# Kernel optimization log

Hardware: AMD Instinct MI355X
Metric: run time of the kernel (lower is better)

The kernel has to match this reference:

```python
import jax, jax.numpy as jnp
import numpy as np

B = 4
MAX_N = 2048
D = 512
H = 8
HD = D // H
SRC_LENS = [2048, 1536, 1800, 1200]   # sum = 6584
REF_LENS = [1900, 2048, 1400, 1600]   # sum = 6948
NEG_INF = -1e9


def setup_inputs() -> dict:
    key = jax.random.key(0)
    ks = jax.random.split(key, 8)
    n_src, n_ref = sum(SRC_LENS), sum(REF_LENS)
    s = 0.02
    return {
        "feats_src": jax.random.normal(ks[0], (n_src, D), dtype=jnp.float32),
        "batch_src": jnp.asarray(np.repeat(np.arange(B), SRC_LENS), dtype=jnp.int32),
        "feats_ref": jax.random.normal(ks[1], (n_ref, D), dtype=jnp.float32),
        "batch_ref": jnp.asarray(np.repeat(np.arange(B), REF_LENS), dtype=jnp.int32),
        "w_in": jax.random.normal(ks[2], (3 * D, D), dtype=jnp.float32) * s,
        "b_in": jnp.zeros((3 * D,), dtype=jnp.float32),
        "w_out": jax.random.normal(ks[3], (D, D), dtype=jnp.float32) * s,
        "b_out": jnp.zeros((D,), dtype=jnp.float32),
        "gw1": jax.random.normal(ks[4], (D, D), dtype=jnp.float32) * s,
        "gb1": jnp.zeros((D,), dtype=jnp.float32),
        "gw2": jax.random.normal(ks[5], (1, D), dtype=jnp.float32) * s,
        "gb2": jnp.zeros((1,), dtype=jnp.float32),
    }


def _to_dense(feats, batch_idx):
    # sparse [N, D] (sorted batch indices) -> dense [B, MAX_N, D] + key_padding_mask
    n = feats.shape[0]
    counts = jax.ops.segment_sum(jnp.ones((n,), jnp.int32), batch_idx, num_segments=B)
    starts = jnp.concatenate([jnp.zeros((1,), jnp.int32), jnp.cumsum(counts)[:-1].astype(jnp.int32)])
    pos = jnp.arange(n, dtype=jnp.int32) - starts[batch_idx]  # position within batch
    dense = jnp.zeros((B, MAX_N, feats.shape[1]), feats.dtype).at[batch_idx, pos].set(feats)
    mask = jnp.arange(MAX_N)[None, :] >= counts[:, None]  # True = padding (key_padding_mask)
    return dense, mask, pos


def reference(feats_src, batch_src, feats_ref, batch_ref,
              w_in, b_in, w_out, b_out, gw1, gb1, gw2, gb2):
    d_src, mask_src, pos_src = _to_dense(feats_src, batch_src)
    d_ref, mask_ref, _ = _to_dense(feats_ref, batch_ref)

    # nn.MultiheadAttention (batch_first, eval mode): packed in_proj, scaled dot-product
    q = (d_src @ w_in[:D].T + b_in[:D]).reshape(B, MAX_N, H, HD)
    k = (d_ref @ w_in[D:2 * D].T + b_in[D:2 * D]).reshape(B, MAX_N, H, HD)
    v = (d_ref @ w_in[2 * D:].T + b_in[2 * D:]).reshape(B, MAX_N, H, HD)
    scores = jnp.einsum('bqhd,bkhd->bhqk', q * (HD ** -0.5), k)
    scores = jnp.where(mask_ref[:, None, None, :], NEG_INF, scores)
    attn = jax.nn.softmax(scores, axis=-1)
    ctx = jnp.einsum('bhqk,bkhd->bqhd', attn, v).reshape(B, MAX_N, D)
    d_aligned = ctx @ w_out.T + b_out

    # gate MLP: Linear -> ReLU -> Linear -> Sigmoid
    gate = jax.nn.sigmoid(jax.nn.relu(d_aligned @ gw1.T + gb1) @ gw2.T + gb2)  # [B, MAX_N, 1]
    d_out = d_src + gate * d_aligned

    # dense -> ragged: gather each token back to its flat slot
    out_flat = d_out[batch_src, pos_src]  # [N_src, D]
    return out_flat, gate
```

## Files before the change

### kernel.cpp

```cpp
#include <hip/hip_runtime.h>
#include <hip/hip_bf16.h>


typedef __bf16 bf16x8_t __attribute__((ext_vector_type(8)));
typedef __bf16 bf16x4_t __attribute__((ext_vector_type(4)));
typedef float f32x4_t __attribute__((ext_vector_type(4)));
typedef float f32x2_t __attribute__((ext_vector_type(2)));

#define CQ_SCALE 0.18033688011112042f

__device__ inline bf16x8_t zero8() {
  bf16x8_t z;
#pragma unroll
  for (int t = 0; t < 8; ++t) z[t] = (__bf16)0.0f;
  return z;
}

__device__ __forceinline__ int sniff_f32(const void* w) {
  unsigned short u = ((const unsigned short*)w)[threadIdx.x & 63];
  return __ballot((u & 0x7F80) >= 0x3F80) != 0ULL;
}

__global__ void sentinel_k(float* out) {
  if (threadIdx.x == 0 && blockIdx.x == 0) out[0] = 1000.0f;
}

__global__ void cv_all(const void* w_in, const void* b_in, const void* w_out,
                       const void* b_out, const void* gw1, const void* gb1,
                       const void* gw2, const void* gb2,
                       __hip_bfloat16* __restrict__ ws) {
  int f = sniff_f32(w_in);
  const size_t F_W_IN = 16, F_B_IN = 786448, F_W_OUT = 787984, F_B_OUT = 1050128,
               F_GW1 = 1050640, F_GB1 = 1312784, F_GW2 = 1313296, F_GB2 = 1313808;
  const int total = 1313793;
  for (int g = blockIdx.x * 256 + threadIdx.x; g < total; g += gridDim.x * 256) {
    const void* src;
    size_t dst;
    int i;
    if (g < 786432) { src = w_in; dst = F_W_IN; i = g; }
    else if (g < 787968) { src = b_in; dst = F_B_IN; i = g - 786432; }
    else if (g < 1050112) { src = w_out; dst = F_W_OUT; i = g - 787968; }
    else if (g < 1050624) { src = b_out; dst = F_B_OUT; i = g - 1050112; }
    else if (g < 1312768) { src = gw1; dst = F_GW1; i = g - 1050624; }
    else if (g < 1313280) { src = gb1; dst = F_GB1; i = g - 1312768; }
    else if (g < 1313792) { src = gw2; dst = F_GW2; i = g - 1313280; }
    else { src = gb2; dst = F_GB2; i = g - 1313792; }
    ws[dst + i] = f ? __float2bfloat16(((const float*)src)[i])
                    : ((const __hip_bfloat16*)src)[i];
  }
}

__device__ __forceinline__ void gemm_core(
    const void* __restrict__ A_, long aoff, const __hip_bfloat16* __restrict__ Bt,
    const __hip_bfloat16* __restrict__ bias, __hip_bfloat16* __restrict__ C,
    int M, int K, int lda, int ldc, float cscale, int relu, int f, int bm, int bn,
    __bf16 (&As)[128][64], __bf16 (&Bs)[128][64]) {
  int tid = threadIdx.x, lane = tid & 63, wave = tid >> 6;
  int wm = wave >> 1, wn = wave & 1;
  int l15 = lane & 15, quad = lane >> 4;

  f32x4_t acc[4][4];
#pragma unroll
  for (int i = 0; i < 4; ++i)
#pragma unroll
    for (int j = 0; j < 4; ++j)
#pragma unroll
      for (int r = 0; r < 4; ++r) acc[i][j][r] = 0.f;

  bf16x8_t ra[4], rb[4];
  f32x4_t raf[4][2];

  auto gload = [&](int k0) {
#pragma unroll
    for (int s = 0; s < 4; ++s) {
      int id = s * 256 + tid;
      int row = id >> 3, col = (id & 7) * 8;
      int arow = bm + row;
      if (f) {
        if (arow < M) {
          const float* p = (const float*)A_ + aoff + (size_t)arow * lda + k0 + col;
          raf[s][0] = *reinterpret_cast<const f32x4_t*>(p);
          raf[s][1] = *reinterpret_cast<const f32x4_t*>(p + 4);
        } else {
#pragma unroll
          for (int e = 0; e < 4; ++e) { raf[s][0][e] = 0.f; raf[s][1][e] = 0.f; }
        }
      } else {
        ra[s] = (arow < M)
                    ? *reinterpret_cast<const bf16x8_t*>((const __hip_bfloat16*)A_ + aoff +
                                                         (size_t)arow * lda + k0 + col)
                    : zero8();
      }
      rb[s] = *reinterpret_cast<const bf16x8_t*>(Bt + (size_t)(bn + row) * 512 + k0 + col);
    }
  };
  auto stage = [&]() {
#pragma unroll
    for (int s = 0; s < 4; ++s) {
      int id = s * 256 + tid;
      int row = id >> 3, col = (id & 7) * 8;
      if (f) {
        bf16x8_t t;
#pragma unroll
        for (int e = 0; e < 4; ++e) {
          t[e] = (__bf16)raf[s][0][e];
          t[4 + e] = (__bf16)raf[s][1][e];
        }
        *reinterpret_cast<bf16x8_t*>(&As[row][col]) = t;
      } else {
        *reinterpret_cast<bf16x8_t*>(&As[row][col]) = ra[s];
      }
      *reinterpret_cast<bf16x8_t*>(&Bs[row][col]) = rb[s];
    }
  };

  int nk = K >> 6;
  gload(0);
  for (int it = 0; it < nk; ++it) {
    stage();
    __syncthreads();
    if (it + 1 < nk) gload((it + 1) * 64);
#pragma unroll
    for (int ks = 0; ks < 2; ++ks) {
      bf16x8_t af[4], bfv[4];
#pragma unroll
      for (int i = 0; i < 4; ++i)
        af[i] = *reinterpret_cast<const bf16x8_t*>(
            &As[wm * 64 + i * 16 + l15][ks * 32 + quad * 8]);
#pragma unroll
      for (int j = 0; j < 4; ++j)
        bfv[j] = *reinterpret_cast<const bf16x8_t*>(
            &Bs[wn * 64 + j * 16 + l15][ks * 32 + quad * 8]);
#pragma unroll
      for (int i = 0; i < 4; ++i)
#pragma unroll
        for (int j = 0; j < 4; ++j)
          acc[i][j] = __builtin_amdgcn_mfma_f32_16x16x32_bf16(af[i], bfv[j], acc[i][j], 0, 0, 0);
    }
    __syncthreads();
  }

#pragma unroll
  for (int i = 0; i < 4; ++i)
#pragma unroll
    for (int j = 0; j < 4; ++j) {
      int col = bn + wn * 64 + j * 16 + l15;
      float bv = __bfloat162float(bias[col]);
#pragma unroll
      for (int r = 0; r < 4; ++r) {
        int row = bm + wm * 64 + i * 16 + quad * 4 + r;
        if (row < M) {
          float v = (acc[i][j][r] + bv) * cscale;
          if (relu) v = fmaxf(v, 0.f);
          C[(size_t)row * ldc + col] = __float2bfloat16(v);
        }
      }
    }
}

__global__ __launch_bounds__(256) void proj2(
    const void* __restrict__ fs, const void* __restrict__ fr,
    const __hip_bfloat16* __restrict__ ws, __hip_bfloat16* __restrict__ Q,
    __hip_bfloat16* __restrict__ KV, const void* snf) {
  __shared__ __bf16 As[128][64];
  __shared__ __bf16 Bs[128][64];
  const size_t F_W_IN = 16, F_B_IN = 786448;
  int f = sniff_f32(snf);
  int bid = blockIdx.x;
  if (bid < 208) {
    int bx = bid >> 2, by = bid & 3;
    gemm_core(fs, 0, ws + F_W_IN, ws + F_B_IN, Q, 6584, 512, 512, 512, CQ_SCALE, 0, f,
              bx * 128, by * 128, As, Bs);
  } else {
    int k = bid - 208;
    int bx = k >> 3, by = k & 7;
    gemm_core(fr, 0, ws + F_W_IN + 262144, ws + F_B_IN + 512, KV, 6948, 512, 512, 1024,
              1.0f, 0, f, bx * 128, by * 128, As, Bs);
  }
}

template <bool AF32>
__global__ __launch_bounds__(256) void gemm128(
    const void* __restrict__ A_, long aoff, const __hip_bfloat16* __restrict__ Bt,
    const __hip_bfloat16* __restrict__ bias, __hip_bfloat16* __restrict__ C,
    int M, int K, int lda, int ldc, float cscale, int relu, const void* snf) {
  __shared__ __bf16 As[128][64];
  __shared__ __bf16 Bs[128][64];
  int f = 0;
  if constexpr (AF32) f = sniff_f32(snf);
  gemm_core(A_, aoff, Bt, bias, C, M, K, lda, ldc, cscale, relu, f,
            blockIdx.x * 128, blockIdx.y * 128, As, Bs);
}

__global__ __launch_bounds__(256) void gemm128_pv(
    const __hip_bfloat16* __restrict__ P0, const __hip_bfloat16* __restrict__ P1,
    const float* __restrict__ L, const __hip_bfloat16* __restrict__ Bt,
    const __hip_bfloat16* __restrict__ bias, __hip_bfloat16* __restrict__ C,
    int M) {
  __shared__ __bf16 As[128][64];
  __shared__ __bf16 Bs[128][64];
  int tid = threadIdx.x, lane = tid & 63, wave = tid >> 6;
  int wm = wave >> 1, wn = wave & 1;
  int l15 = lane & 15, quad = lane >> 4;
  int bm = blockIdx.x * 128, bn = blockIdx.y * 128;

  f32x4_t acc[4][4];
#pragma unroll
  for (int i = 0; i < 4; ++i)
#pragma unroll
    for (int j = 0; j < 4; ++j)
#pragma unroll
      for (int r = 0; r < 4; ++r) acc[i][j][r] = 0.f;

  bf16x8_t rp0[4], rp1[4], rb[4];
  f32x2_t rl[4];

  auto gload = [&](int k0) {
    int h = k0 >> 6;
#pragma unroll
    for (int s = 0; s < 4; ++s) {
      int id = s * 256 + tid;
      int row = id >> 3, col = (id & 7) * 8;
      int arow = bm + row;
      if (arow < M) {
        size_t off = (size_t)arow * 512 + k0 + col;
        rp0[s] = *reinterpret_cast<const bf16x8_t*>(P0 + off);
        rp1[s] = *reinterpret_cast<const bf16x8_t*>(P1 + off);
        rl[s] = *reinterpret_cast<const f32x2_t*>(&L[((size_t)arow * 8 + h) * 2]);
      } else {
        rp0[s] = zero8();
        rp1[s] = zero8();
        rl[s][0] = 1.f;
        rl[s][1] = 0.f;
      }
      rb[s] = *reinterpret_cast<const bf16x8_t*>(Bt + (size_t)(bn + row) * 512 + k0 + col);
    }
  };
  auto stage = [&]() {
#pragma unroll
    for (int s = 0; s < 4; ++s) {
      int id = s * 256 + tid;
      int row = id >> 3, col = (id & 7) * 8;
      float sc = 1.0f / (rl[s][0] + rl[s][1]);
      float w0 = rl[s][0] * sc, w1 = rl[s][1] * sc;
      bf16x8_t t;
#pragma unroll
      for (int e = 0; e < 8; ++e)
        t[e] = (__bf16)(w0 * (float)rp0[s][e] + w1 * (float)rp1[s][e]);
      *reinterpret_cast<bf16x8_t*>(&As[row][col]) = t;
      *reinterpret_cast<bf16x8_t*>(&Bs[row][col]) = rb[s];
    }
  };

  gload(0);
  for (int it = 0; it < 8; ++it) {
    stage();
    __syncthreads();
    if (it + 1 < 8) gload((it + 1) * 64);
#pragma unroll
    for (int ks = 0; ks < 2; ++ks) {
      bf16x8_t af[4], bfv[4];
#pragma unroll
      for (int i = 0; i < 4; ++i)
        af[i] = *reinterpret_cast<const bf16x8_t*>(
            &As[wm * 64 + i * 16 + l15][ks * 32 + quad * 8]);
#pragma unroll
      for (int j = 0; j < 4; ++j)
        bfv[j] = *reinterpret_cast<const bf16x8_t*>(
            &Bs[wn * 64 + j * 16 + l15][ks * 32 + quad * 8]);
#pragma unroll
      for (int i = 0; i < 4; ++i)
#pragma unroll
        for (int j = 0; j < 4; ++j)
          acc[i][j] = __builtin_amdgcn_mfma_f32_16x16x32_bf16(af[i], bfv[j], acc[i][j], 0, 0, 0);
    }
    __syncthreads();
  }

#pragma unroll
  for (int i = 0; i < 4; ++i)
#pragma unroll
    for (int j = 0; j < 4; ++j) {
      int col = bn + wn * 64 + j * 16 + l15;
      float bv = __bfloat162float(bias[col]);
#pragma unroll
      for (int r = 0; r < 4; ++r) {
        int row = bm + wm * 64 + i * 16 + quad * 4 + r;
        if (row < M)
          C[(size_t)row * 512 + col] = __float2bfloat16(acc[i][j][r] + bv);
      }
    }
}

__device__ __forceinline__ void flash_core(
    const __hip_bfloat16* __restrict__ Qb, const __hip_bfloat16* __restrict__ KVb,
    __hip_bfloat16* __restrict__ OUTb, float* __restrict__ LPb, int nsrc, int nref,
    int qt, int kt0, int ktNfull, int do_tail,
    __bf16 (&VtL)[2][64][72], __bf16 (&PL)[4][32][72]) {
  int h = blockIdx.y;
  int tid = threadIdx.x, lane = tid & 63, wave = tid >> 6;
  int l15 = lane & 15, quad = lane >> 4;
  int Mb = nsrc + 1;
  int qbase = qt * 128 + wave * 32;

  bf16x8_t qfr[2][2];
#pragma unroll
  for (int g = 0; g < 2; ++g) {
    int qrow = qbase + g * 16 + l15;
#pragma unroll
    for (int ks = 0; ks < 2; ++ks)
      qfr[g][ks] = (qrow < nsrc)
                       ? *reinterpret_cast<const bf16x8_t*>(
                             Qb + (size_t)qrow * 512 + h * 64 + ks * 32 + quad * 8)
                       : zero8();
  }

  f32x4_t O[2][4];
#pragma unroll
  for (int g = 0; g < 2; ++g)
#pragma unroll
    for (int j = 0; j < 4; ++j)
#pragma unroll
      for (int r = 0; r < 4; ++r) O[g][j][r] = 0.f;

  f32x4_t Lacc[2];
#pragma unroll
  for (int g = 0; g < 2; ++g)
#pragma unroll
    for (int r = 0; r < 4; ++r) Lacc[g][r] = 0.f;
  bf16x8_t ones;
#pragma unroll
  for (int t = 0; t < 8; ++t) ones[t] = (__bf16)1.0f;

  bf16x8_t kf[8], v0, v1;
  auto loadK = [&](int k0) {
#pragma unroll
    for (int j = 0; j < 4; ++j) {
      const __hip_bfloat16* kp =
          KVb + (size_t)(k0 + j * 16 + l15) * 1024 + h * 64 + quad * 8;
      kf[j * 2] = *reinterpret_cast<const bf16x8_t*>(kp);
      kf[j * 2 + 1] = *reinterpret_cast<const bf16x8_t*>(kp + 32);
    }
  };
  auto loadV = [&](int k0) {
    const __hip_bfloat16* vp = KVb + (size_t)(k0 + lane) * 1024 + 512 + h * 64 + wave * 16;
    v0 = *reinterpret_cast<const bf16x8_t*>(vp);
    v1 = *reinterpret_cast<const bf16x8_t*>(vp + 8);
  };

  int nit = ktNfull - kt0;
  if (nit > 0) {
    loadK(kt0 * 64);
    loadV(kt0 * 64);
  }

  for (int it = 0; it < nit; ++it) {
    int k0 = (kt0 + it) * 64;
    __bf16(*Vt)[72] = VtL[it & 1];
#pragma unroll
    for (int e = 0; e < 8; ++e) {
      Vt[wave * 16 + e][lane] = v0[e];
      Vt[wave * 16 + 8 + e][lane] = v1[e];
    }
    if (it + 1 < nit) loadV(k0 + 64);

#pragma unroll
    for (int g = 0; g < 2; ++g) {
      f32x4_t St[4];
#pragma unroll
      for (int j = 0; j < 4; ++j)
#pragma unroll
        for (int r = 0; r < 4; ++r) St[j][r] = 0.f;
#pragma unroll
      for (int j = 0; j < 4; ++j)
#pragma unroll
        for (int ks = 0; ks < 2; ++ks)
          St[j] = __builtin_amdgcn_mfma_f32_16x16x32_bf16(kf[j * 2 + ks], qfr[g][ks],
                                                          St[j], 0, 0, 0);
#pragma unroll
      for (int j = 0; j < 4; ++j) {
        bf16x4_t pk;
#pragma unroll
        for (int r = 0; r < 4; ++r) pk[r] = (__bf16)exp2f(St[j][r]);
        *reinterpret_cast<bf16x4_t*>(&PL[wave][g * 16 + l15][j * 16 + quad * 4]) = pk;
      }
    }
    if (it + 1 < nit) loadK(k0 + 64);

    __syncthreads();

    bf16x8_t pa[2][2];
#pragma unroll
    for (int g = 0; g < 2; ++g)
#pragma unroll
      for (int ks = 0; ks < 2; ++ks)
        pa[g][ks] = *reinterpret_cast<const bf16x8_t*>(
            &PL[wave][g * 16 + l15][ks * 32 + quad * 8]);
#pragma unroll
    for (int g = 0; g < 2; ++g)
#pragma unroll
      for (int ks = 0; ks < 2; ++ks)
        Lacc[g] = __builtin_amdgcn_mfma_f32_16x16x32_bf16(pa[g][ks], ones, Lacc[g], 0, 0, 0);
#pragma unroll
    for (int j = 0; j < 4; ++j)
#pragma unroll
      for (int ks = 0; ks < 2; ++ks) {
        bf16x8_t vbf =
            *reinterpret_cast<const bf16x8_t*>(&Vt[j * 16 + l15][ks * 32 + quad * 8]);
#pragma unroll
        for (int g = 0; g < 2; ++g)
          O[g][j] = __builtin_amdgcn_mfma_f32_16x16x32_bf16(pa[g][ks], vbf, O[g][j], 0, 0, 0);
      }
  }

  if (do_tail) {
    int k0 = ktNfull * 64;
    __bf16(*Vt)[72] = VtL[nit & 1];
    {
      int kr = k0 + lane;
      const __hip_bfloat16* vp = KVb + (size_t)kr * 1024 + 512 + h * 64 + wave * 16;
      bf16x8_t t0 = (kr < nref) ? *reinterpret_cast<const bf16x8_t*>(vp) : zero8();
      bf16x8_t t1 = (kr < nref) ? *reinterpret_cast<const bf16x8_t*>(vp + 8) : zero8();
#pragma unroll
      for (int e = 0; e < 8; ++e) {
        Vt[wave * 16 + e][lane] = t0[e];
        Vt[wave * 16 + 8 + e][lane] = t1[e];
      }
    }
#pragma unroll
    for (int j = 0; j < 4; ++j) {
      int kcol = k0 + j * 16 + l15;
      const __hip_bfloat16* kp = KVb + (size_t)kcol * 1024 + h * 64 + quad * 8;
      kf[j * 2] = (kcol < nref) ? *reinterpret_cast<const bf16x8_t*>(kp) : zero8();
      kf[j * 2 + 1] = (kcol < nref) ? *reinterpret_cast<const bf16x8_t*>(kp + 32) : zero8();
    }
#pragma unroll
    for (int g = 0; g < 2; ++g) {
      f32x4_t St[4];
#pragma unroll
      for (int j = 0; j < 4; ++j)
#pragma unroll
        for (int r = 0; r < 4; ++r) St[j][r] = 0.f;
#pragma unroll
      for (int j = 0; j < 4; ++j)
#pragma unroll
        for (int ks = 0; ks < 2; ++ks)
          St[j] = __builtin_amdgcn_mfma_f32_16x16x32_bf16(kf[j * 2 + ks], qfr[g][ks],
                                                          St[j], 0, 0, 0);
#pragma unroll
      for (int j = 0; j < 4; ++j) {
        bf16x4_t pk;
#pragma unroll
        for (int r = 0; r < 4; ++r) {
          int kl = k0 + j * 16 + quad * 4 + r;
          pk[r] = (__bf16)((kl < nref) ? exp2f(St[j][r]) : 0.f);
        }
        *reinterpret_cast<bf16x4_t*>(&PL[wave][g * 16 + l15][j * 16 + quad * 4]) = pk;
      }
    }
    __syncthreads();
    bf16x8_t pa[2][2];
#pragma unroll
    for (int g = 0; g < 2; ++g)
#pragma unroll
      for (int ks = 0; ks < 2; ++ks)
        pa[g][ks] = *reinterpret_cast<const bf16x8_t*>(
            &PL[wave][g * 16 + l15][ks * 32 + quad * 8]);
#pragma unroll
    for (int g = 0; g < 2; ++g)
#pragma unroll
      for (int ks = 0; ks < 2; ++ks)
        Lacc[g] = __builtin_amdgcn_mfma_f32_16x16x32_bf16(pa[g][ks], ones, Lacc[g], 0, 0, 0);
#pragma unroll
    for (int j = 0; j < 4; ++j)
#pragma unroll
      for (int ks = 0; ks < 2; ++ks) {
        bf16x8_t vbf =
            *reinterpret_cast<const bf16x8_t*>(&Vt[j * 16 + l15][ks * 32 + quad * 8]);
#pragma unroll
        for (int g = 0; g < 2; ++g)
          O[g][j] = __builtin_amdgcn_mfma_f32_16x16x32_bf16(pa[g][ks], vbf, O[g][j], 0, 0, 0);
      }
  }

  if (LPb && l15 == 0) {
#pragma unroll
    for (int g = 0; g < 2; ++g)
#pragma unroll
      for (int r = 0; r < 4; ++r) {
        int row = qbase + g * 16 + quad * 4 + r;
        if (row < Mb) LPb[((size_t)row * 8 + h) * 2] = Lacc[g][r];
      }
  }

#pragma unroll
  for (int g = 0; g < 2; ++g)
#pragma unroll
    for (int r = 0; r < 4; ++r) {
      int row = qbase + g * 16 + quad * 4 + r;
      if (row < Mb) {
        float inv = 1.0f / Lacc[g][r];
#pragma unroll
        for (int j = 0; j < 4; ++j)
          OUTb[(size_t)row * 512 + h * 64 + j * 16 + l15] =
              __float2bfloat16(O[g][j][r] * inv);
      }
    }
}

__global__ __launch_bounds__(256, 3) void flash_all(
    const __hip_bfloat16* __restrict__ Q, const __hip_bfloat16* __restrict__ KV,
    __hip_bfloat16* __restrict__ O0, __hip_bfloat16* __restrict__ O1,
    float* __restrict__ L, int nsplit) {
  const int TILE_START[4] = {0, 17, 30, 45};
  const int SRC_START[4] = {0, 2048, 3584, 5384};
  const int REF_START[4] = {0, 1900, 3948, 5348};
  const int SRC_LEN[4] = {2048, 1536, 1800, 1200};
  const int REF_LEN[4] = {1900, 2048, 1400, 1600};
  const int CS[4] = {0, 2049, 3586, 5387};
  __shared__ __bf16 VtL[2][64][72];
  __shared__ __bf16 PL[4][32][72];
  int bid = blockIdx.x;
  int b = (bid >= TILE_START[3]) ? 3 : (bid >= TILE_START[2]) ? 2 : (bid >= TILE_START[1]) ? 1 : 0;
  int qt = bid - TILE_START[b];
  int nref = REF_LEN[b];
  int full = nref >> 6, nkt = (nref + 63) >> 6, rem = nref & 63;
  int split = blockIdx.z;
  int kt0, ktN, tail;
  if (nsplit == 1) { kt0 = 0; ktN = full; tail = rem > 0; }
  else if (split == 0) { int half = nkt >> 1; kt0 = 0; ktN = half; tail = 0; }
  else { int half = nkt >> 1; kt0 = half; ktN = full; tail = rem > 0; }
  __hip_bfloat16* OUT = (nsplit == 1 || split == 0) ? O0 : O1;
  float* LP = (nsplit == 1) ? nullptr : (L + split + (size_t)CS[b] * 16);
  flash_core(Q + (size_t)SRC_START[b] * 512, KV + (size_t)REF_START[b] * 1024,
             OUT + (size_t)CS[b] * 512, LP, SRC_LEN[b], nref, qt, kt0, ktN, tail, VtL, PL);
}

__global__ __launch_bounds__(256, 3) void flash_one(const __hip_bfloat16* __restrict__ Qb,
                                                    const __hip_bfloat16* __restrict__ KVb,
                                                    __hip_bfloat16* __restrict__ OUTb,
                                                    int nsrc, int nref) {
  __shared__ __bf16 VtL[2][64][72];
  __shared__ __bf16 PL[4][32][72];
  flash_core(Qb, KVb, OUTb, nullptr, nsrc, nref, blockIdx.x, 0, nref >> 6,
             (nref & 63) > 0, VtL, PL);
}

__global__ __launch_bounds__(256) void finalize_all(
    const void* __restrict__ src, const __hip_bfloat16* __restrict__ aligned,
    const __hip_bfloat16* __restrict__ hidden, const __hip_bfloat16* __restrict__ gw2,
    const __hip_bfloat16* __restrict__ gb2, void* __restrict__ out, const void* snf) {
  int f = sniff_f32(snf);
  int lane = threadIdx.x & 63;
  int r = blockIdx.x * 4 + (threadIdx.x >> 6);
  int b = (r >= 5387) ? 3 : (r >= 3586) ? 2 : (r >= 2049) ? 1 : 0;
  const int CS[4] = {0, 2049, 3586, 5387};
  const int NSRC[4] = {2048, 1536, 1800, 1200};
  int pos = r - CS[b];

  float zacc = 0.f;
  const __hip_bfloat16* hrow = hidden + (size_t)r * 512;
#pragma unroll
  for (int t = 0; t < 8; ++t) {
    int c = lane + (t << 6);
    zacc += __bfloat162float(hrow[c]) * __bfloat162float(gw2[c]);
  }
  for (int o = 32; o; o >>= 1) zacc += __shfl_xor(zacc, o);
  zacc += __bfloat162float(gb2[0]);
  float g = 1.f / (1.f + __expf(-zacc));

  const size_t GOFF = (size_t)6584 * 512;
  if (pos < NSRC[b]) {
    size_t ib = (size_t)(r - b) * 512;
    const __hip_bfloat16* arow = aligned + (size_t)r * 512;
#pragma unroll
    for (int t = 0; t < 8; ++t) {
      int c = lane + (t << 6);
      float sv = f ? ((const float*)src)[ib + c]
                   : __bfloat162float(((const __hip_bfloat16*)src)[ib + c]);
      float val = sv + g * __bfloat162float(arow[c]);
      if (f) ((float*)out)[ib + c] = val;
      else ((__hip_bfloat16*)out)[ib + c] = __float2bfloat16(val);
    }
    if (lane == 0) {
      size_t go = GOFF + b * 2048 + pos;
      if (f) ((float*)out)[go] = g;
      else ((__hip_bfloat16*)out)[go] = __float2bfloat16(g);
    }
  } else {
    for (int p = NSRC[b] + lane; p < 2048; p += 64) {
      size_t go = GOFF + b * 2048 + p;
      if (f) ((float*)out)[go] = g;
      else ((__hip_bfloat16*)out)[go] = __float2bfloat16(g);
    }
  }
}

__global__ __launch_bounds__(256) void finalize_b(
    const void* __restrict__ src, const __hip_bfloat16* __restrict__ alnb,
    const __hip_bfloat16* __restrict__ hidb, const __hip_bfloat16* __restrict__ gw2,
    const __hip_bfloat16* __restrict__ gb2, void* __restrict__ out,
    int b, int nsrc, int src_start, const void* snf) {
  int f = sniff_f32(snf);
  int lane = threadIdx.x & 63;
  int r = blockIdx.x * 4 + (threadIdx.x >> 6);
  if (r > nsrc) return;

  float zacc = 0.f;
  const __hip_bfloat16* hrow = hidb + (size_t)r * 512;
#pragma unroll
  for (int t = 0; t < 8; ++t) {
    int c = lane + (t << 6);
    zacc += __bfloat162float(hrow[c]) * __bfloat162float(gw2[c]);
  }
  for (int o = 32; o; o >>= 1) zacc += __shfl_xor(zacc, o);
  zacc += __bfloat162float(gb2[0]);
  float g = 1.f / (1.f + __expf(-zacc));

  const size_t GOFF = (size_t)6584 * 512;
  if (r < nsrc) {
    size_t ib = (size_t)(src_start + r) * 512;
    const __hip_bfloat16* arow = alnb + (size_t)r * 512;
#pragma unroll
    for (int t = 0; t < 8; ++t) {
      int c = lane + (t << 6);
      float sv = f ? ((const float*)src)[ib + c]
                   : __bfloat162float(((const __hip_bfloat16*)src)[ib + c]);
      float val = sv + g * __bfloat162float(arow[c]);
      if (f) ((float*)out)[ib + c] = val;
      else ((__hip_bfloat16*)out)[ib + c] = __float2bfloat16(val);
    }
    if (lane == 0) {
      size_t go = GOFF + b * 2048 + r;
      if (f) ((float*)out)[go] = g;
      else ((__hip_bfloat16*)out)[go] = __float2bfloat16(g);
    }
  } else {
    for (int p = nsrc + lane; p < 2048; p += 64) {
      size_t go = GOFF + b * 2048 + p;
      if (f) ((float*)out)[go] = g;
      else ((__hip_bfloat16*)out)[go] = __float2bfloat16(g);
    }
  }
}

extern "C" void kernel_launch(void* const* d_in, const int* in_sizes, int n_in,
                              void* d_out, int out_size, void* d_ws, size_t ws_size,
                              hipStream_t stream) {
  (void)in_sizes; (void)n_in; (void)out_size;
  const void* feats_src = d_in[0];
  const void* feats_ref = d_in[2];
  const void* w_in = d_in[4];
  const void* b_in = d_in[5];
  const void* w_out = d_in[6];
  const void* b_out = d_in[7];
  const void* gw1 = d_in[8];
  const void* gb1 = d_in[9];
  const void* gw2 = d_in[10];
  const void* gb2 = d_in[11];

  const size_t F_W_IN = 16, F_B_IN = 786448, F_W_OUT = 787984, F_B_OUT = 1050128,
               F_GW1 = 1050640, F_GB1 = 1312784, F_GW2 = 1313296, F_GB2 = 1313808,
               A0 = 1313824;
  const size_t NEED_A2 = 2 * 22139936;
  const size_t NEED_A = 2 * 15178784;
  const size_t NEED_B = 2 * (A0 + 4259840);

  if (ws_size < NEED_B) {
    sentinel_k<<<1, 64, 0, stream>>>((float*)d_out);
    return;
  }

  __hip_bfloat16* ws = (__hip_bfloat16*)d_ws;
  cv_all<<<dim3(1024), dim3(256), 0, stream>>>(w_in, b_in, w_out, b_out, gw1, gb1, gw2,
                                               gb2, ws);

  const int SRC_LEN[4] = {2048, 1536, 1800, 1200};
  const int REF_LEN[4] = {1900, 2048, 1400, 1600};
  const int SRC_START[4] = {0, 2048, 3584, 5384};
  const int REF_START[4] = {0, 1900, 3948, 5348};
  dim3 blk(256);

  if (ws_size >= NEED_A) {
    __hip_bfloat16* R1 = ws + A0;
    __hip_bfloat16* R2 = R1 + 3375104;
    __hip_bfloat16* R3 = R2 + 7114752;
    proj2<<<dim3(648), blk, 0, stream>>>(feats_src, feats_ref, ws, R1, R2, w_in);
    if (ws_size >= NEED_A2) {
      __hip_bfloat16* P0 = R3 + 3375104;
      __hip_bfloat16* P1 = P0 + 3375104;
      float* L = (float*)(ws + 21928992);
      flash_all<<<dim3(55, 8, 2), blk, 0, stream>>>(R1, R2, P0, P1, L, 2);
      gemm128_pv<<<dim3(52, 4), blk, 0, stream>>>(P0, P1, L, ws + F_W_OUT, ws + F_B_OUT,
                                                  R1, 6588);
    } else {
      flash_all<<<dim3(55, 8, 1), blk, 0, stream>>>(R1, R2, R3, nullptr, nullptr, 1);
      gemm128<false><<<dim3(52, 4), blk, 0, stream>>>(R3, 0, ws + F_W_OUT, ws + F_B_OUT,
                                                      R1, 6588, 512, 512, 512, 1.0f, 0,
                                                      nullptr);
    }
    gemm128<false><<<dim3(52, 4), blk, 0, stream>>>(R1, 0, ws + F_GW1, ws + F_GB1, R3,
                                                    6588, 512, 512, 512, 1.0f, 1,
                                                    nullptr);
    finalize_all<<<dim3(1647), blk, 0, stream>>>(feats_src, R1, R3, ws + F_GW2,
                                                 ws + F_GB2, d_out, w_in);
  } else {
    __hip_bfloat16* W2 = ws + A0;
    __hip_bfloat16* W1 = W2 + 2097152;
    __hip_bfloat16* W3 = W1 + 1081344;
    for (int b = 0; b < 4; ++b) {
      int nsrc = SRC_LEN[b], nref = REF_LEN[b];
      gemm128<true><<<dim3((nsrc + 127) / 128, 4), blk, 0, stream>>>(
          feats_src, (long)SRC_START[b] * 512, ws + F_W_IN, ws + F_B_IN, W1, nsrc, 512,
          512, 512, CQ_SCALE, 0, w_in);
      gemm128<true><<<dim3((nref + 127) / 128, 8), blk, 0, stream>>>(
          feats_ref, (long)REF_START[b] * 512, ws + F_W_IN + 262144, ws + F_B_IN + 512,
          W2, nref, 512, 512, 1024, 1.0f, 0, w_in);
      flash_one<<<dim3((nsrc + 128) / 128, 8), blk, 0, stream>>>(W1, W2, W3, nsrc, nref);
      gemm128<false><<<dim3((nsrc + 128) / 128, 4), blk, 0, stream>>>(
          W3, 0, ws + F_W_OUT, ws + F_B_OUT, W1, nsrc + 1, 512, 512, 512, 1.0f, 0,
          nullptr);
      gemm128<false><<<dim3((nsrc + 128) / 128, 4), blk, 0, stream>>>(
          W1, 0, ws + F_GW1, ws + F_GB1, W3, nsrc + 1, 512, 512, 512, 1.0f, 1, nullptr);
      finalize_b<<<dim3((nsrc + 4) / 4), blk, 0, stream>>>(
          feats_src, W1, W3, ws + F_GW2, ws + F_GB2, d_out, b, nsrc, SRC_START[b], w_in);
    }
  }
}
```

Measured before the change: 256.6 us.

## Generalize flash-decoding KV split to four splits with templated merge GEMM

Flash attention now splits the key range into NS parts (4 when workspace allows, else 2 or 1), writing partial outputs and row sums into contiguous slabs. The out-projection GEMM is templated on NS and merges the partial outputs, weighted by their row sums, while staging its A tile. Launch bounds on the flash kernels rise from 3 to 4 waves per SIMD to raise occupancy. More splits add parallelism (55x8x4 blocks), but they also add partial-output traffic and merge work, and register pressure may spill under the tighter launch bound.

```diff
diff --git a/kernel.cpp b/kernel.cpp
--- a/kernel.cpp
+++ b/kernel.cpp
@@ -192,11 +192,12 @@
             blockIdx.x * 128, blockIdx.y * 128, As, Bs);
 }
 
+template <int NS>
 __global__ __launch_bounds__(256) void gemm128_pv(
-    const __hip_bfloat16* __restrict__ P0, const __hip_bfloat16* __restrict__ P1,
-    const float* __restrict__ L, const __hip_bfloat16* __restrict__ Bt,
-    const __hip_bfloat16* __restrict__ bias, __hip_bfloat16* __restrict__ C,
-    int M) {
+    const __hip_bfloat16* __restrict__ P, const float* __restrict__ L,
+    const __hip_bfloat16* __restrict__ Bt, const __hip_bfloat16* __restrict__ bias,
+    __hip_bfloat16* __restrict__ C, int M) {
+  const size_t PSZ = 3375104;
   __shared__ __bf16 As[128][64];
   __shared__ __bf16 Bs[128][64];
   int tid = threadIdx.x, lane = tid & 63, wave = tid >> 6;
@@ -212,8 +213,8 @@
 #pragma unroll
       for (int r = 0; r < 4; ++r) acc[i][j][r] = 0.f;
 
-  bf16x8_t rp0[4], rp1[4], rb[4];
-  f32x2_t rl[4];
+  bf16x8_t rp[NS][4], rb[4];
+  float rl[4][NS];
 
   auto gload = [&](int k0) {
     int h = k0 >> 6;
@@ -224,14 +225,18 @@
       int arow = bm + row;
       if (arow < M) {
         size_t off = (size_t)arow * 512 + k0 + col;
-        rp0[s] = *reinterpret_cast<const bf16x8_t*>(P0 + off);
-        rp1[s] = *reinterpret_cast<const bf16x8_t*>(P1 + off);
-        rl[s] = *reinterpret_cast<const f32x2_t*>(&L[((size_t)arow * 8 + h) * 2]);
+#pragma unroll
+        for (int i = 0; i < NS; ++i)
+          rp[i][s] = *reinterpret_cast<const bf16x8_t*>(P + i * PSZ + off);
+        const float* lp = &L[((size_t)arow * 8 + h) * NS];
+#pragma unroll
+        for (int i = 0; i < NS; ++i) rl[s][i] = lp[i];
       } else {
-        rp0[s] = zero8();
-        rp1[s] = zero8();
+#pragma unroll
+        for (int i = 0; i < NS; ++i) rp[i][s] = zero8();
         rl[s][0] = 1.f;
-        rl[s][1] = 0.f;
+#pragma unroll
+        for (int i = 1; i < NS; ++i) rl[s][i] = 0.f;
       }
       rb[s] = *reinterpret_cast<const bf16x8_t*>(Bt + (size_t)(bn + row) * 512 + k0 + col);
     }
@@ -241,12 +246,18 @@
     for (int s = 0; s < 4; ++s) {
       int id = s * 256 + tid;
       int row = id >> 3, col = (id & 7) * 8;
-      float sc = 1.0f / (rl[s][0] + rl[s][1]);
-      float w0 = rl[s][0] * sc, w1 = rl[s][1] * sc;
+      float sum = 0.f;
+#pragma unroll
+      for (int i = 0; i < NS; ++i) sum += rl[s][i];
+      float sc = 1.0f / sum;
       bf16x8_t t;
 #pragma unroll
-      for (int e = 0; e < 8; ++e)
-        t[e] = (__bf16)(w0 * (float)rp0[s][e] + w1 * (float)rp1[s][e]);
+      for (int e = 0; e < 8; ++e) {
+        float v = 0.f;
+#pragma unroll
+        for (int i = 0; i < NS; ++i) v += rl[s][i] * (float)rp[i][s][e];
+        t[e] = (__bf16)(v * sc);
+      }
       *reinterpret_cast<bf16x8_t*>(&As[row][col]) = t;
       *reinterpret_cast<bf16x8_t*>(&Bs[row][col]) = rb[s];
     }
@@ -294,8 +305,8 @@
 
 __device__ __forceinline__ void flash_core(
     const __hip_bfloat16* __restrict__ Qb, const __hip_bfloat16* __restrict__ KVb,
-    __hip_bfloat16* __restrict__ OUTb, float* __restrict__ LPb, int nsrc, int nref,
-    int qt, int kt0, int ktNfull, int do_tail,
+    __hip_bfloat16* __restrict__ OUTb, float* __restrict__ LPb, int lns,
+    int nsrc, int nref, int qt, int kt0, int ktNfull, int do_tail,
     __bf16 (&VtL)[2][64][72], __bf16 (&PL)[4][32][72]) {
   int h = blockIdx.y;
   int tid = threadIdx.x, lane = tid & 63, wave = tid >> 6;
@@ -489,7 +500,7 @@
 #pragma unroll
       for (int r = 0; r < 4; ++r) {
         int row = qbase + g * 16 + quad * 4 + r;
-        if (row < Mb) LPb[((size_t)row * 8 + h) * 2] = Lacc[g][r];
+        if (row < Mb) LPb[((size_t)row * 8 + h) * lns] = Lacc[g][r];
       }
   }
 
@@ -508,16 +519,16 @@
     }
 }
 
-__global__ __launch_bounds__(256, 3) void flash_all(
+__global__ __launch_bounds__(256, 4) void flash_all(
     const __hip_bfloat16* __restrict__ Q, const __hip_bfloat16* __restrict__ KV,
-    __hip_bfloat16* __restrict__ O0, __hip_bfloat16* __restrict__ O1,
-    float* __restrict__ L, int nsplit) {
+    __hip_bfloat16* __restrict__ P, float* __restrict__ L, int nsplit) {
   const int TILE_START[4] = {0, 17, 30, 45};
   const int SRC_START[4] = {0, 2048, 3584, 5384};
   const int REF_START[4] = {0, 1900, 3948, 5348};
   const int SRC_LEN[4] = {2048, 1536, 1800, 1200};
   const int REF_LEN[4] = {1900, 2048, 1400, 1600};
   const int CS[4] = {0, 2049, 3586, 5387};
+  const size_t PSZ = 3375104;
   __shared__ __bf16 VtL[2][64][72];
   __shared__ __bf16 PL[4][32][72];
   int bid = blockIdx.x;
@@ -526,23 +537,24 @@
   int nref = REF_LEN[b];
   int full = nref >> 6, nkt = (nref + 63) >> 6, rem = nref & 63;
   int split = blockIdx.z;
-  int kt0, ktN, tail;
-  if (nsplit == 1) { kt0 = 0; ktN = full; tail = rem > 0; }
-  else if (split == 0) { int half = nkt >> 1; kt0 = 0; ktN = half; tail = 0; }
-  else { int half = nkt >> 1; kt0 = half; ktN = full; tail = rem > 0; }
-  __hip_bfloat16* OUT = (nsplit == 1 || split == 0) ? O0 : O1;
-  float* LP = (nsplit == 1) ? nullptr : (L + split + (size_t)CS[b] * 16);
+  int kt0 = (nkt * split) / nsplit;
+  int ktN, tail;
+  if (split == nsplit - 1) { ktN = full; tail = rem > 0; }
+  else { ktN = (nkt * (split + 1)) / nsplit; tail = 0; }
+  __hip_bfloat16* OUT = P + (size_t)split * PSZ;
+  float* LP = (nsplit == 1) ? nullptr : (L + split + (size_t)CS[b] * 8 * nsplit);
   flash_core(Q + (size_t)SRC_START[b] * 512, KV + (size_t)REF_START[b] * 1024,
-             OUT + (size_t)CS[b] * 512, LP, SRC_LEN[b], nref, qt, kt0, ktN, tail, VtL, PL);
-}
-
-__global__ __launch_bounds__(256, 3) void flash_one(const __hip_bfloat16* __restrict__ Qb,
+             OUT + (size_t)CS[b] * 512, LP, nsplit, SRC_LEN[b], nref, qt, kt0, ktN,
+             tail, VtL, PL);
+}
+
+__global__ __launch_bounds__(256, 4) void flash_one(const __hip_bfloat16* __restrict__ Qb,
                                                     const __hip_bfloat16* __restrict__ KVb,
                                                     __hip_bfloat16* __restrict__ OUTb,
                                                     int nsrc, int nref) {
   __shared__ __bf16 VtL[2][64][72];
   __shared__ __bf16 PL[4][32][72];
-  flash_core(Qb, KVb, OUTb, nullptr, nsrc, nref, blockIdx.x, 0, nref >> 6,
+  flash_core(Qb, KVb, OUTb, nullptr, 1, nsrc, nref, blockIdx.x, 0, nref >> 6,
              (nref & 63) > 0, VtL, PL);
 }
 
@@ -662,8 +674,11 @@
   const size_t F_W_IN = 16, F_B_IN = 786448, F_W_OUT = 787984, F_B_OUT = 1050128,
                F_GW1 = 1050640, F_GB1 = 1312784, F_GW2 = 1313296, F_GB2 = 1313808,
                A0 = 1313824;
-  const size_t NEED_A2 = 2 * 22139936;
-  const size_t NEED_A = 2 * 15178784;
+  const size_t PSZ = 3375104;
+  const size_t R3E = A0 + PSZ + 7114752;
+  const size_t NEED_A4 = 2 * (R3E + 4 * PSZ + 421632);
+  const size_t NEED_A2 = 2 * (R3E + 2 * PSZ + 210816);
+  const size_t NEED_A = 2 * (R3E + PSZ);
   const size_t NEED_B = 2 * (A0 + 4259840);
 
   if (ws_size < NEED_B) {
@@ -683,18 +698,21 @@
 
   if (ws_size >= NEED_A) {
     __hip_bfloat16* R1 = ws + A0;
-    __hip_bfloat16* R2 = R1 + 3375104;
+    __hip_bfloat16* R2 = R1 + PSZ;
     __hip_bfloat16* R3 = R2 + 7114752;
     proj2<<<dim3(648), blk, 0, stream>>>(feats_src, feats_ref, ws, R1, R2, w_in);
-    if (ws_size >= NEED_A2) {
-      __hip_bfloat16* P0 = R3 + 3375104;
-      __hip_bfloat16* P1 = P0 + 3375104;
-      float* L = (float*)(ws + 21928992);
-      flash_all<<<dim3(55, 8, 2), blk, 0, stream>>>(R1, R2, P0, P1, L, 2);
-      gemm128_pv<<<dim3(52, 4), blk, 0, stream>>>(P0, P1, L, ws + F_W_OUT, ws + F_B_OUT,
-                                                  R1, 6588);
+    int NS = (ws_size >= NEED_A4) ? 4 : (ws_size >= NEED_A2) ? 2 : 1;
+    if (NS >= 2) {
+      float* L = (float*)(ws + R3E + (size_t)NS * PSZ);
+      flash_all<<<dim3(55, 8, NS), blk, 0, stream>>>(R1, R2, R3, L, NS);
+      if (NS == 4)
+        gemm128_pv<4><<<dim3(52, 4), blk, 0, stream>>>(R3, L, ws + F_W_OUT,
+                                                       ws + F_B_OUT, R1, 6588);
+      else
+        gemm128_pv<2><<<dim3(52, 4), blk, 0, stream>>>(R3, L, ws + F_W_OUT,
+                                                       ws + F_B_OUT, R1, 6588);
     } else {
-      flash_all<<<dim3(55, 8, 1), blk, 0, stream>>>(R1, R2, R3, nullptr, nullptr, 1);
+      flash_all<<<dim3(55, 8, 1), blk, 0, stream>>>(R1, R2, R3, nullptr, 1);
       gemm128<false><<<dim3(52, 4), blk, 0, stream>>>(R3, 0, ws + F_W_OUT, ws + F_B_OUT,
                                                       R1, 6588, 512, 512, 512, 1.0f, 0,
                                                       nullptr);
```

Result: slower. 268.4 us (+4.6%).
